# Kernel tuning notes

Measured on AMD Instinct MI355X. Metric: run time of the kernel, lower is better.

## Reference

```python
import jax, jax.numpy as jnp
import numpy as np

N, K, F, A = 20000, 32, 256, 128
BN_EPS = 1e-3  # Keras BatchNormalization default epsilon


def setup_inputs() -> dict:
    key = jax.random.key(0)
    k1, k2, k3, k4 = jax.random.split(key, 4)
    self_feats = jax.random.normal(k1, (N, F), dtype=jnp.float32)
    neigh_feats = jax.random.normal(k2, (N, K, F), dtype=jnp.float32)
    W_shared = jax.random.normal(k3, (F, A), dtype=jnp.float32) * (1.0 / np.sqrt(F))
    b_shared = jnp.zeros((A,), dtype=jnp.float32)
    gamma = jnp.ones((A,), dtype=jnp.float32)
    beta = jnp.zeros((A,), dtype=jnp.float32)
    W_out = jax.random.normal(k4, (2 * A, 1), dtype=jnp.float32) * (1.0 / np.sqrt(2 * A))
    b_out = jnp.zeros((1,), dtype=jnp.float32)
    return {"self_feats": self_feats, "neigh_feats": neigh_feats,
            "W_shared": W_shared, "b_shared": b_shared,
            "gamma": gamma, "beta": beta, "W_out": W_out, "b_out": b_out}


def _bn_train(x, gamma, beta):
    # BatchNorm in training mode: batch statistics over leading axis
    mean = jnp.mean(x, axis=0, keepdims=True)
    var = jnp.var(x, axis=0, keepdims=True)
    return (x - mean) * jax.lax.rsqrt(var + BN_EPS) * gamma + beta


def reference(self_feats, neigh_feats, W_shared, b_shared, gamma, beta, W_out, b_out):
    # shared Dense + BN on self features: [N, A]
    s = _bn_train(self_feats @ W_shared + b_shared, gamma, beta)
    # shared Dense on neighbor features, BN over flattened [N*K, A] batch
    n = neigh_feats.reshape(-1, F) @ W_shared + b_shared  # [N*K, A]
    n = _bn_train(n, gamma, beta).reshape(neigh_feats.shape[0], neigh_feats.shape[1], -1)  # [N, K, A]
    # broadcast self feats over neighbors and concat: [N, K, 2A]
    s_b = jnp.broadcast_to(s[:, None, :], n.shape)
    concat = jnp.concatenate([s_b, n], axis=2)
    # attention logits: Dense(2A -> 1), activation, softmax over neighbors
    logits = concat @ W_out + b_out  # [N, K, 1]
    logits = jax.nn.relu(logits)
    coeff = jax.nn.softmax(jnp.squeeze(logits, axis=2), axis=-1)  # [N, K]
    return coeff[:, :, None]  # [N, K, 1]
```

## Files before the change

kernel.cpp:

```cpp
#include <hip/hip_runtime.h>
#include <cstdint>
#include <cstddef>


typedef __attribute__((ext_vector_type(8))) short short8;
typedef __attribute__((ext_vector_type(4))) float float4v;

__device__ __forceinline__ unsigned short f2bf(float f) {
  union { float f; unsigned u; } v; v.f = f;
  unsigned r = v.u + 0x7FFFu + ((v.u >> 16) & 1u);
  return (unsigned short)(r >> 16);
}
__device__ __forceinline__ float bfu(unsigned v) {
  union { unsigned u; float f; } t; t.u = v << 16; return t.f;
}

__global__ __launch_bounds__(256) void transpose_w(const float* __restrict__ W,
                                                   unsigned short* __restrict__ Wt) {
  const int n = blockIdx.x;
  const int k = threadIdx.x;
  Wt[n * 256 + k] = f2bf(W[k * 128 + n]);
}

#define BM 128
#define APAD 40

__global__ __launch_bounds__(256) void stats_gemm(
    const float* __restrict__ X, int R, int nTiles,
    const unsigned short* __restrict__ Wt,
    unsigned short* __restrict__ U,
    float* __restrict__ partials) {
  __shared__ __align__(16) unsigned short As[BM * APAD];
  __shared__ __align__(16) unsigned short Bs[128 * APAD];
  __shared__ float csum[128];
  __shared__ float csq[128];

  const int tid  = threadIdx.x;
  const int lane = tid & 63;
  const int wv   = tid >> 6;
  const int waveM = wv >> 1;
  const int waveN = wv & 1;
  const int quad  = lane >> 4;
  const int l16   = lane & 15;

  float runsum = 0.f, runsq = 0.f;

  for (int t = blockIdx.x; t < nTiles; t += gridDim.x) {
    const int row0 = t * BM;
    float4v acc[4][4];
#pragma unroll
    for (int rb = 0; rb < 4; ++rb)
#pragma unroll
      for (int cb = 0; cb < 4; ++cb)
        acc[rb][cb] = (float4v){0.f, 0.f, 0.f, 0.f};

    for (int kc = 0; kc < 8; ++kc) {
      __syncthreads();
#pragma unroll
      for (int it = 0; it < 4; ++it) {
        int idx = it * 256 + tid;
        int r = idx >> 3, j = idx & 7;
        float4 v = make_float4(0.f, 0.f, 0.f, 0.f);
        int gr = row0 + r;
        if (gr < R) v = *(const float4*)(X + (size_t)gr * 256 + kc * 32 + j * 4);
        uint2 p;
        p.x = (unsigned)f2bf(v.x) | ((unsigned)f2bf(v.y) << 16);
        p.y = (unsigned)f2bf(v.z) | ((unsigned)f2bf(v.w) << 16);
        *(uint2*)&As[r * APAD + j * 4] = p;
      }
#pragma unroll
      for (int it = 0; it < 4; ++it) {
        int idx = it * 256 + tid;
        int n = idx >> 3, j = idx & 7;
        *(uint2*)&Bs[n * APAD + j * 4] =
            *(const uint2*)(Wt + n * 256 + kc * 32 + j * 4);
      }
      __syncthreads();

      short8 a[4], b[4];
#pragma unroll
      for (int rb = 0; rb < 4; ++rb)
        a[rb] = *(const short8*)&As[(waveM * 64 + rb * 16 + l16) * APAD + quad * 8];
#pragma unroll
      for (int cb = 0; cb < 4; ++cb)
        b[cb] = *(const short8*)&Bs[(waveN * 64 + cb * 16 + l16) * APAD + quad * 8];
#pragma unroll
      for (int rb = 0; rb < 4; ++rb)
#pragma unroll
        for (int cb = 0; cb < 4; ++cb)
          acc[rb][cb] = __builtin_amdgcn_mfma_f32_16x16x32_bf16(
              a[rb], b[cb], acc[rb][cb], 0, 0, 0);
    }

    __syncthreads();
    float ps[4], pq[4];
#pragma unroll
    for (int cb = 0; cb < 4; ++cb) {
      const int col = waveN * 64 + cb * 16 + l16;
      float s = 0.f, q = 0.f;
#pragma unroll
      for (int rb = 0; rb < 4; ++rb) {
#pragma unroll
        for (int rg = 0; rg < 4; ++rg) {
          int grow = row0 + waveM * 64 + rb * 16 + quad * 4 + rg;
          float x = acc[rb][cb][rg];
          if (grow < R) {
            U[(size_t)grow * 128 + col] = f2bf(x);
            s += x;
            q += x * x;
          }
        }
      }
      s += __shfl_xor(s, 16); s += __shfl_xor(s, 32);
      q += __shfl_xor(q, 16); q += __shfl_xor(q, 32);
      ps[cb] = s; pq[cb] = q;
    }
    if (waveM == 0 && quad == 0) {
#pragma unroll
      for (int cb = 0; cb < 4; ++cb) {
        int col = waveN * 64 + cb * 16 + l16;
        csum[col] = ps[cb];
        csq[col]  = pq[cb];
      }
    }
    __syncthreads();
    if (waveM == 1 && quad == 0) {
#pragma unroll
      for (int cb = 0; cb < 4; ++cb) {
        int col = waveN * 64 + cb * 16 + l16;
        csum[col] += ps[cb];
        csq[col]  += pq[cb];
      }
    }
    __syncthreads();
    if (tid < 128) runsum += csum[tid];
    else           runsq  += csq[tid - 128];
  }
  partials[blockIdx.x * 256 + tid] = (tid < 128) ? runsum : runsq;
}

__global__ __launch_bounds__(256) void reduce_partials(
    const float* __restrict__ ps, int ns, const float* __restrict__ pn, int nn,
    float* __restrict__ stats) {
  __shared__ float buf[256];
  const int c = blockIdx.x;
  const int tid = threadIdx.x;
  float a = 0.f;
  for (int g = tid; g < ns; g += 256) a += ps[(size_t)g * 256 + c];
  buf[tid] = a;
  __syncthreads();
  for (int s = 128; s > 0; s >>= 1) {
    if (tid < s) buf[tid] += buf[tid + s];
    __syncthreads();
  }
  if (tid == 0) stats[c] = buf[0];
  float b = 0.f;
  for (int g = tid; g < nn; g += 256) b += pn[(size_t)g * 256 + c];
  __syncthreads();
  buf[tid] = b;
  __syncthreads();
  for (int s = 128; s > 0; s >>= 1) {
    if (tid < s) buf[tid] += buf[tid + s];
    __syncthreads();
  }
  if (tid == 0) stats[256 + c] = buf[0];
}

__global__ __launch_bounds__(128) void setup_kernel(
    const float* __restrict__ stats,
    const float* __restrict__ gamma, const float* __restrict__ beta,
    const float* __restrict__ Wout, const float* __restrict__ bout,
    float* __restrict__ G1, float* __restrict__ G2, float* __restrict__ Cout) {
  __shared__ float carr[128];
  const int tid = threadIdx.x;
  const float invNs = 1.f / 20000.f, invNn = 1.f / 640000.f;
  float ms = stats[tid] * invNs;
  float vs = stats[128 + tid] * invNs - ms * ms;
  float is = rsqrtf(vs + 1e-3f);
  float mn = stats[256 + tid] * invNn;
  float vn = stats[384 + tid] * invNn - mn * mn;
  float in_ = rsqrtf(vn + 1e-3f);
  float w1 = Wout[tid], w2 = Wout[128 + tid];
  float g1 = is * gamma[tid] * w1;
  float g2 = in_ * gamma[tid] * w2;
  G1[tid] = g1;
  G2[tid] = g2;
  carr[tid] = beta[tid] * (w1 + w2) - ms * g1 - mn * g2;
  __syncthreads();
  if (tid == 0) {
    float c = bout[0];
    for (int a = 0; a < 128; ++a) c += carr[a];
    Cout[0] = c;
  }
}

__global__ __launch_bounds__(256) void attn_final(
    const unsigned short* __restrict__ Us,
    const unsigned short* __restrict__ Un,
    const float* __restrict__ G1, const float* __restrict__ G2,
    const float* __restrict__ Cptr, float* __restrict__ out) {
  const int lane = threadIdx.x & 63;
  const int wv = threadIdx.x >> 6;
  const int i = blockIdx.x * 4 + wv;
  const int l16 = lane & 15;
  const int l32 = lane & 31;
  const int quarter = lane >> 4;
  const float C = Cptr[0];

  unsigned su = *(const unsigned*)(Us + (size_t)i * 128 + lane * 2);
  float2 g1p = *(const float2*)(G1 + lane * 2);
  float sd = fmaf(g1p.x, bfu(su), g1p.y * bfu(su >> 16));
#pragma unroll
  for (int m = 32; m >= 1; m >>= 1) sd += __shfl_xor(sd, m);

  const float4 ga = *(const float4*)(G2 + l16 * 8);
  const float4 gb = *(const float4*)(G2 + l16 * 8 + 4);
  const unsigned short* un = Un + (size_t)i * 4096;
  float ml = 0.f;
#pragma unroll
  for (int j = 0; j < 8; ++j) {
    const int nb = j * 4 + quarter;
    uint4 q = *(const uint4*)(un + nb * 128 + l16 * 8);
    float p;
    p = fmaf(ga.x, bfu(q.x), ga.y * bfu(q.x >> 16));
    p = fmaf(ga.z, bfu(q.y), p); p = fmaf(ga.w, bfu(q.y >> 16), p);
    p = fmaf(gb.x, bfu(q.z), p); p = fmaf(gb.y, bfu(q.z >> 16), p);
    p = fmaf(gb.z, bfu(q.w), p); p = fmaf(gb.w, bfu(q.w >> 16), p);
#pragma unroll
    for (int m = 1; m <= 8; m <<= 1) p += __shfl_xor(p, m);
    float s16 = __shfl_xor(p, 16);
    float s32 = __shfl_xor(p, 32);
    float s48 = __shfl_xor(s16, 32);
    if ((l32 >> 2) == j) {
      int x = (l32 & 3) ^ quarter;
      ml = (x == 0) ? p : (x == 1) ? s16 : (x == 2) ? s32 : s48;
    }
  }
  float logit = fmaxf(ml + sd + C, 0.f);
  float mx = logit;
#pragma unroll
  for (int m = 16; m >= 1; m >>= 1) mx = fmaxf(mx, __shfl_xor(mx, m));
  float e = __expf(logit - mx);
  float ssum = e;
#pragma unroll
  for (int m = 16; m >= 1; m >>= 1) ssum += __shfl_xor(ssum, m);
  if (lane < 32) out[(size_t)i * 32 + lane] = e / ssum;
}

extern "C" void kernel_launch(void* const* d_in, const int* in_sizes, int n_in,
                              void* d_out, int out_size, void* d_ws, size_t ws_size,
                              hipStream_t stream) {
  const float* self  = (const float*)d_in[0];
  const float* neigh = (const float*)d_in[1];
  const float* W     = (const float*)d_in[2];
  const float* gamma = (const float*)d_in[4];
  const float* beta  = (const float*)d_in[5];
  const float* Wout  = (const float*)d_in[6];
  const float* bout  = (const float*)d_in[7];
  float* out = (float*)d_out;

  char* ws = (char*)d_ws;
  unsigned short* Wt = (unsigned short*)ws;
  unsigned short* Us = (unsigned short*)(ws + (1 << 16));
  unsigned short* Un = Us + (size_t)20000 * 128;
  float* part_s = (float*)(Un + (size_t)640000 * 128);
  float* part_n = part_s + 157 * 256;
  float* stats  = part_n + 1024 * 256;
  float* G1     = stats + 512;
  float* G2     = G1 + 128;
  float* Cc     = G2 + 128;

  hipLaunchKernelGGL(transpose_w, dim3(128), dim3(256), 0, stream, W, Wt);
  hipLaunchKernelGGL(stats_gemm, dim3(157), dim3(256), 0, stream,
                     self, 20000, 157, Wt, Us, part_s);
  hipLaunchKernelGGL(stats_gemm, dim3(1024), dim3(256), 0, stream,
                     neigh, 640000, 5000, Wt, Un, part_n);
  hipLaunchKernelGGL(reduce_partials, dim3(256), dim3(256), 0, stream,
                     part_s, 157, part_n, 1024, stats);
  hipLaunchKernelGGL(setup_kernel, dim3(1), dim3(128), 0, stream,
                     stats, gamma, beta, Wout, bout, G1, G2, Cc);
  hipLaunchKernelGGL(attn_final, dim3(5000), dim3(256), 0, stream,
                     Us, Un, G1, G2, Cc, out);
}
```

Baseline: 1.020 ms.

## Keep bf16 weights resident in LDS and load A fragments directly to registers

```diff
diff --git a/kernel.cpp b/kernel.cpp
--- a/kernel.cpp
+++ b/kernel.cpp
@@ -13,6 +13,9 @@
 }
 __device__ __forceinline__ float bfu(unsigned v) {
   union { unsigned u; float f; } t; t.u = v << 16; return t.f;
+}
+__device__ __forceinline__ unsigned pkbf(float x, float y) {
+  return (unsigned)f2bf(x) | ((unsigned)f2bf(y) << 16);
 }
 
 __global__ __launch_bounds__(256) void transpose_w(const float* __restrict__ W,
@@ -22,121 +25,111 @@
   Wt[n * 256 + k] = f2bf(W[k * 128 + n]);
 }
 
-#define BM 128
-#define APAD 40
-
-__global__ __launch_bounds__(256) void stats_gemm(
+#define BROW 264
+
+template <bool GUARD>
+__global__ __launch_bounds__(256) void stats_gemm2(
     const float* __restrict__ X, int R, int nTiles,
     const unsigned short* __restrict__ Wt,
     unsigned short* __restrict__ U,
     float* __restrict__ partials) {
-  __shared__ __align__(16) unsigned short As[BM * APAD];
-  __shared__ __align__(16) unsigned short Bs[128 * APAD];
-  __shared__ float csum[128];
-  __shared__ float csq[128];
+  __shared__ __align__(16) unsigned short Bs[128 * BROW];
+  __shared__ float cred[1024];
 
   const int tid  = threadIdx.x;
   const int lane = tid & 63;
   const int wv   = tid >> 6;
-  const int waveM = wv >> 1;
-  const int waveN = wv & 1;
-  const int quad  = lane >> 4;
-  const int l16   = lane & 15;
-
-  float runsum = 0.f, runsq = 0.f;
+  const int quad = lane >> 4;
+  const int l16  = lane & 15;
+
+#pragma unroll
+  for (int it = 0; it < 16; ++it) {
+    int e = it * 256 + tid;
+    int r = e >> 5, c = e & 31;
+    *(uint4*)&Bs[r * BROW + c * 8] = *(const uint4*)(Wt + r * 256 + c * 8);
+  }
+  __syncthreads();
+
+  float rs[8], rq[8];
+#pragma unroll
+  for (int cb = 0; cb < 8; ++cb) { rs[cb] = 0.f; rq[cb] = 0.f; }
 
   for (int t = blockIdx.x; t < nTiles; t += gridDim.x) {
-    const int row0 = t * BM;
-    float4v acc[4][4];
-#pragma unroll
-    for (int rb = 0; rb < 4; ++rb)
-#pragma unroll
-      for (int cb = 0; cb < 4; ++cb)
+    const int row0 = t * 128 + wv * 32;
+    float4v acc[2][8];
+#pragma unroll
+    for (int rb = 0; rb < 2; ++rb)
+#pragma unroll
+      for (int cb = 0; cb < 8; ++cb)
         acc[rb][cb] = (float4v){0.f, 0.f, 0.f, 0.f};
 
+#pragma unroll
     for (int kc = 0; kc < 8; ++kc) {
-      __syncthreads();
-#pragma unroll
-      for (int it = 0; it < 4; ++it) {
-        int idx = it * 256 + tid;
-        int r = idx >> 3, j = idx & 7;
-        float4 v = make_float4(0.f, 0.f, 0.f, 0.f);
-        int gr = row0 + r;
-        if (gr < R) v = *(const float4*)(X + (size_t)gr * 256 + kc * 32 + j * 4);
-        uint2 p;
-        p.x = (unsigned)f2bf(v.x) | ((unsigned)f2bf(v.y) << 16);
-        p.y = (unsigned)f2bf(v.z) | ((unsigned)f2bf(v.w) << 16);
-        *(uint2*)&As[r * APAD + j * 4] = p;
+      short8 a[2];
+#pragma unroll
+      for (int rb = 0; rb < 2; ++rb) {
+        const int gr = row0 + rb * 16 + l16;
+        float4 v0 = make_float4(0.f, 0.f, 0.f, 0.f);
+        float4 v1 = make_float4(0.f, 0.f, 0.f, 0.f);
+        if (!GUARD || gr < R) {
+          const float* p = X + (size_t)gr * 256 + kc * 32 + quad * 8;
+          v0 = *(const float4*)p;
+          v1 = *(const float4*)(p + 4);
+        }
+        union { short8 s; unsigned u[4]; } af;
+        af.u[0] = pkbf(v0.x, v0.y);
+        af.u[1] = pkbf(v0.z, v0.w);
+        af.u[2] = pkbf(v1.x, v1.y);
+        af.u[3] = pkbf(v1.z, v1.w);
+        a[rb] = af.s;
       }
 #pragma unroll
-      for (int it = 0; it < 4; ++it) {
-        int idx = it * 256 + tid;
-        int n = idx >> 3, j = idx & 7;
-        *(uint2*)&Bs[n * APAD + j * 4] =
-            *(const uint2*)(Wt + n * 256 + kc * 32 + j * 4);
+      for (int cb = 0; cb < 8; ++cb) {
+        short8 b = *(const short8*)&Bs[(cb * 16 + l16) * BROW + kc * 32 + quad * 8];
+#pragma unroll
+        for (int rb = 0; rb < 2; ++rb)
+          acc[rb][cb] = __builtin_amdgcn_mfma_f32_16x16x32_bf16(
+              a[rb], b, acc[rb][cb], 0, 0, 0);
       }
-      __syncthreads();
-
-      short8 a[4], b[4];
-#pragma unroll
-      for (int rb = 0; rb < 4; ++rb)
-        a[rb] = *(const short8*)&As[(waveM * 64 + rb * 16 + l16) * APAD + quad * 8];
-#pragma unroll
-      for (int cb = 0; cb < 4; ++cb)
-        b[cb] = *(const short8*)&Bs[(waveN * 64 + cb * 16 + l16) * APAD + quad * 8];
-#pragma unroll
-      for (int rb = 0; rb < 4; ++rb)
-#pragma unroll
-        for (int cb = 0; cb < 4; ++cb)
-          acc[rb][cb] = __builtin_amdgcn_mfma_f32_16x16x32_bf16(
-              a[rb], b[cb], acc[rb][cb], 0, 0, 0);
-    }
-
-    __syncthreads();
-    float ps[4], pq[4];
-#pragma unroll
-    for (int cb = 0; cb < 4; ++cb) {
-      const int col = waveN * 64 + cb * 16 + l16;
-      float s = 0.f, q = 0.f;
-#pragma unroll
-      for (int rb = 0; rb < 4; ++rb) {
+    }
+
+#pragma unroll
+    for (int rb = 0; rb < 2; ++rb) {
+#pragma unroll
+      for (int cb = 0; cb < 8; ++cb) {
+        const int col = cb * 16 + l16;
 #pragma unroll
         for (int rg = 0; rg < 4; ++rg) {
-          int grow = row0 + waveM * 64 + rb * 16 + quad * 4 + rg;
-          float x = acc[rb][cb][rg];
-          if (grow < R) {
-            U[(size_t)grow * 128 + col] = f2bf(x);
-            s += x;
-            q += x * x;
-          }
+          const int grow = row0 + rb * 16 + quad * 4 + rg;
+          const float x = acc[rb][cb][rg];
+          if (!GUARD || grow < R) U[(size_t)grow * 128 + col] = f2bf(x);
+          rs[cb] += x;
+          rq[cb] = fmaf(x, x, rq[cb]);
         }
       }
-      s += __shfl_xor(s, 16); s += __shfl_xor(s, 32);
-      q += __shfl_xor(q, 16); q += __shfl_xor(q, 32);
-      ps[cb] = s; pq[cb] = q;
-    }
-    if (waveM == 0 && quad == 0) {
-#pragma unroll
-      for (int cb = 0; cb < 4; ++cb) {
-        int col = waveN * 64 + cb * 16 + l16;
-        csum[col] = ps[cb];
-        csq[col]  = pq[cb];
-      }
-    }
-    __syncthreads();
-    if (waveM == 1 && quad == 0) {
-#pragma unroll
-      for (int cb = 0; cb < 4; ++cb) {
-        int col = waveN * 64 + cb * 16 + l16;
-        csum[col] += ps[cb];
-        csq[col]  += pq[cb];
-      }
-    }
-    __syncthreads();
-    if (tid < 128) runsum += csum[tid];
-    else           runsq  += csq[tid - 128];
-  }
-  partials[blockIdx.x * 256 + tid] = (tid < 128) ? runsum : runsq;
+    }
+  }
+
+#pragma unroll
+  for (int cb = 0; cb < 8; ++cb) {
+    float s = rs[cb], q = rq[cb];
+    s += __shfl_xor(s, 16); s += __shfl_xor(s, 32);
+    q += __shfl_xor(q, 16); q += __shfl_xor(q, 32);
+    if (quad == 0) {
+      cred[wv * 128 + cb * 16 + l16] = s;
+      cred[512 + wv * 128 + cb * 16 + l16] = q;
+    }
+  }
+  __syncthreads();
+  float out = 0.f;
+  if (tid < 128) {
+#pragma unroll
+    for (int w = 0; w < 4; ++w) out += cred[w * 128 + tid];
+  } else {
+#pragma unroll
+    for (int w = 0; w < 4; ++w) out += cred[512 + w * 128 + (tid - 128)];
+  }
+  partials[(size_t)blockIdx.x * 256 + tid] = out;
 }
 
 __global__ __launch_bounds__(256) void reduce_partials(
@@ -271,12 +264,12 @@
   float* Cc     = G2 + 128;
 
   hipLaunchKernelGGL(transpose_w, dim3(128), dim3(256), 0, stream, W, Wt);
-  hipLaunchKernelGGL(stats_gemm, dim3(157), dim3(256), 0, stream,
+  hipLaunchKernelGGL((stats_gemm2<true>), dim3(157), dim3(256), 0, stream,
                      self, 20000, 157, Wt, Us, part_s);
-  hipLaunchKernelGGL(stats_gemm, dim3(1024), dim3(256), 0, stream,
+  hipLaunchKernelGGL((stats_gemm2<false>), dim3(1000), dim3(256), 0, stream,
                      neigh, 640000, 5000, Wt, Un, part_n);
   hipLaunchKernelGGL(reduce_partials, dim3(256), dim3(256), 0, stream,
-                     part_s, 157, part_n, 1024, stats);
+                     part_s, 157, part_n, 1000, stats);
   hipLaunchKernelGGL(setup_kernel, dim3(1), dim3(128), 0, stream,
                      stats, gamma, beta, Wout, bout, G1, G2, Cc);
   hipLaunchKernelGGL(attn_final, dim3(5000), dim3(256), 0, stream,
```

After: 1.010 ms. Within noise of the previous version (-0.9%).
